# Kernel optimization log

Hardware: AMD Instinct MI355X
Metric: run time of the kernel (lower is better)

## Reference

```python
import jax, jax.numpy as jnp
import numpy as np

N, T = 1024, 32
D_FEAT, GATE_START, GATE_END = 158, 158, 221
D_MODEL = 256
T_NHEAD, S_NHEAD = 4, 2
BETA = 5.0
LN_EPS = 1e-5


def _ln(x, g, b):
    mu = jnp.mean(x, axis=-1, keepdims=True)
    var = jnp.mean(jnp.square(x - mu), axis=-1, keepdims=True)
    return (x - mu) * jax.lax.rsqrt(var + LN_EPS) * g + b


def _pos_enc(t, d):
    pos = jnp.arange(t, dtype=jnp.float32)[:, None]
    div = jnp.exp(jnp.arange(0, d, 2, dtype=jnp.float32) * (-np.log(10000.0) / d))
    pe = jnp.zeros((t, d), dtype=jnp.float32)
    pe = pe.at[:, 0::2].set(jnp.sin(pos * div))
    pe = pe.at[:, 1::2].set(jnp.cos(pos * div))
    return pe


def _mha(xn, qw, kw, vw, nhead, temperature):
    # xn: [B, S, D] (already layer-normed); attention over axis S
    B, S, D = xn.shape
    dh = D // nhead
    q = (xn @ qw.T).reshape(B, S, nhead, dh)
    k = (xn @ kw.T).reshape(B, S, nhead, dh)
    v = (xn @ vw.T).reshape(B, S, nhead, dh)
    scores = jnp.einsum('bshd,bthd->bhst', q, k) / temperature
    a = jax.nn.softmax(scores, axis=-1)
    return jnp.einsum('bhst,bthd->bshd', a, v).reshape(B, S, D)


def _block(x, qw, kw, vw, n1g, n1b, n2g, n2b, f1w, f1b, f2w, f2b, nhead, temperature):
    xn = _ln(x, n1g, n1b)
    xt = xn + _mha(xn, qw, kw, vw, nhead, temperature)
    xt = _ln(xt, n2g, n2b)
    ffn = jnp.maximum(xt @ f1w.T + f1b, 0.0) @ f2w.T + f2b
    return xt + ffn


def _forward(x, gate_w, gate_b, proj_w, proj_b,
             tq, tk, tv, tn1g, tn1b, tn2g, tn2b, tf1w, tf1b, tf2w, tf2b,
             sq, sk, sv, sn1g, sn1b, sn2g, sn2b, sf1w, sf1b, sf2w, sf2b,
             temp_w, out_w, out_b):
    src = x[:, :, :GATE_START]                     # [N, T, d_feat]
    gate_in = x[:, -1, GATE_START:GATE_END]        # [N, d_gate]
    gate = D_FEAT * jax.nn.softmax((gate_in @ gate_w.T + gate_b) / BETA, axis=-1)
    src = src * gate[:, None, :]
    z = src @ proj_w.T + proj_b                    # [N, T, d_model]
    z = z + _pos_enc(z.shape[1], D_MODEL)
    # TAttention: attend over time, unscaled scores (temperature=1)
    z = _block(z, tq, tk, tv, tn1g, tn1b, tn2g, tn2b, tf1w, tf1b, tf2w, tf2b,
               T_NHEAD, 1.0)
    # SAttention: attend over stocks, temperature = sqrt(d_model/nhead)
    zs = _block(z.swapaxes(0, 1), sq, sk, sv, sn1g, sn1b, sn2g, sn2b,
                sf1w, sf1b, sf2w, sf2b, S_NHEAD, float(np.sqrt(D_MODEL / S_NHEAD)))
    z = zs.swapaxes(0, 1)                          # [N, T, d_model]
    # TemporalAttention pooling
    h = z @ temp_w.T
    lam = jax.nn.softmax(jnp.einsum('ntd,nd->nt', h, h[:, -1, :]), axis=1)
    pooled = jnp.einsum('nt,ntd->nd', lam, z)
    return (pooled @ out_w.T + out_b).squeeze(-1)  # [N]


def setup_inputs() -> dict:
    key = jax.random.key(0)
    ks = iter(jax.random.split(key, 32))
    s = 0.02
    d, f, g = D_MODEL, D_FEAT, GATE_END - GATE_START
    inp = {
        'x': jax.random.normal(next(ks), (N, T, GATE_END), dtype=jnp.float32),
        'gate_w': jax.random.normal(next(ks), (f, g)) * s,
        'gate_b': jnp.zeros((f,)),
        'proj_w': jax.random.normal(next(ks), (d, f)) * s,
        'proj_b': jnp.zeros((d,)),
        'tq': jax.random.normal(next(ks), (d, d)) * s,
        'tk': jax.random.normal(next(ks), (d, d)) * s,
        'tv': jax.random.normal(next(ks), (d, d)) * s,
        'tn1g': jnp.ones((d,)), 'tn1b': jnp.zeros((d,)),
        'tn2g': jnp.ones((d,)), 'tn2b': jnp.zeros((d,)),
        'tf1w': jax.random.normal(next(ks), (d, d)) * s, 'tf1b': jnp.zeros((d,)),
        'tf2w': jax.random.normal(next(ks), (d, d)) * s, 'tf2b': jnp.zeros((d,)),
        'sq': jax.random.normal(next(ks), (d, d)) * s,
        'sk': jax.random.normal(next(ks), (d, d)) * s,
        'sv': jax.random.normal(next(ks), (d, d)) * s,
        'sn1g': jnp.ones((d,)), 'sn1b': jnp.zeros((d,)),
        'sn2g': jnp.ones((d,)), 'sn2b': jnp.zeros((d,)),
        'sf1w': jax.random.normal(next(ks), (d, d)) * s, 'sf1b': jnp.zeros((d,)),
        'sf2w': jax.random.normal(next(ks), (d, d)) * s, 'sf2b': jnp.zeros((d,)),
        'temp_w': jax.random.normal(next(ks), (d, d)) * s,
        'out_w': jax.random.normal(next(ks), (1, d)) * s,
        'out_b': jnp.zeros((1,)),
    }
    return {k: v.astype(jnp.float32) for k, v in inp.items()}


def reference(x, gate_w, gate_b, proj_w, proj_b,
              tq, tk, tv, tn1g, tn1b, tn2g, tn2b, tf1w, tf1b, tf2w, tf2b,
              sq, sk, sv, sn1g, sn1b, sn2g, sn2b, sf1w, sf1b, sf2w, sf2b,
              temp_w, out_w, out_b):
    return _forward(x, gate_w, gate_b, proj_w, proj_b,
                    tq, tk, tv, tn1g, tn1b, tn2g, tn2b, tf1w, tf1b, tf2w, tf2b,
                    sq, sk, sv, sn1g, sn1b, sn2g, sn2b, sf1w, sf1b, sf2w, sf2b,
                    temp_w, out_w, out_b)
```

## Files before the change

kernel.cpp:

```cpp
#include <hip/hip_runtime.h>
#include <math.h>

#define NB   1024
#define TSEQ 32
#define DM   256
#define DF   158
#define GDIM 63
#define XROW 221

typedef unsigned short u16;
typedef __attribute__((ext_vector_type(8))) __bf16 bf16x8;
typedef __attribute__((ext_vector_type(4))) float f32x4;
#define MFMA16(a,b,c) __builtin_amdgcn_mfma_f32_16x16x32_bf16(a,b,c,0,0,0)

#define MODE_PROJ 0
#define MODE_QKVT 1
#define MODE_QKVS 2
#define MODE_TEMP 3

__device__ __forceinline__ u16 f2bf(float f){
  union { float f; unsigned int u; } c; c.f = f;
  unsigned int u = c.u;
  u += 0x7fffu + ((u >> 16) & 1u);
  return (u16)(u >> 16);
}

__device__ __forceinline__ void ln_rows32(float* buf, int stride,
                                          const float* __restrict__ g,
                                          const float* __restrict__ b,
                                          int tid)
{
  const int s = tid >> 3, j = tid & 7;
  float* row = buf + s * stride;
  float sum = 0.f, sq = 0.f;
  #pragma unroll
  for (int k = 0; k < DM; k += 8){
    float v = row[k + j];
    sum += v; sq += v * v;
  }
  #pragma unroll
  for (int o = 1; o < 8; o <<= 1){
    sum += __shfl_xor(sum, o);
    sq  += __shfl_xor(sq, o);
  }
  const float mu  = sum * (1.f / DM);
  const float var = sq * (1.f / DM) - mu * mu;
  const float rs  = rsqrtf(var + 1e-5f);
  #pragma unroll
  for (int k = 0; k < DM; k += 8){
    float v = row[k + j];
    row[k + j] = (v - mu) * rs * g[k + j] + b[k + j];
  }
}

#define WB_TOT 770048

__global__ __launch_bounds__(256) void kConvAll(
    const float* __restrict__ tq, const float* __restrict__ tk, const float* __restrict__ tv,
    const float* __restrict__ sq, const float* __restrict__ sk, const float* __restrict__ sv,
    const float* __restrict__ tf1, const float* __restrict__ tf2,
    const float* __restrict__ sf1, const float* __restrict__ sf2,
    const float* __restrict__ tw, const float* __restrict__ pw,
    u16* __restrict__ WB)
{
  int i = blockIdx.x * 256 + threadIdx.x;
  if (i >= WB_TOT) return;
  if (i < 720896){
    int j = i >> 16, o = i & 65535;
    const float* s;
    switch (j){
      case 0: s = tq; break;  case 1: s = tk; break;  case 2: s = tv; break;
      case 3: s = sq; break;  case 4: s = sk; break;  case 5: s = sv; break;
      case 6: s = tf1; break; case 7: s = tf2; break;
      case 8: s = sf1; break; case 9: s = sf2; break;
      default: s = tw; break;
    }
    WB[i] = f2bf(s[o]);
  } else {
    int k = i - 720896;
    int row = k / 192, col = k - row * 192;
    WB[i] = (col < DF) ? f2bf(pw[row * DF + col]) : (u16)0;
  }
}


__global__ __launch_bounds__(256) void kGateSrc(
    const float* __restrict__ x,
    const float* __restrict__ gate_w, const float* __restrict__ gate_b,
    u16* __restrict__ SRC)
{
  __shared__ float s_gate[DF];
  __shared__ float s_gi[GDIM];
  const int tid = threadIdx.x;
  const int n = blockIdx.x;

  if (tid < GDIM) s_gi[tid] = x[(n * TSEQ + (TSEQ - 1)) * XROW + DF + tid];
  __syncthreads();
  float logit = 0.f;
  if (tid < DF){
    logit = gate_b[tid];
    const float* __restrict__ wr = gate_w + tid * GDIM;
    for (int g = 0; g < GDIM; ++g) logit += s_gi[g] * wr[g];
    logit *= 0.2f;
    s_gate[tid] = logit;
  }
  __syncthreads();
  {
    float mx = -1e30f;
    for (int f = 0; f < DF; ++f) mx = fmaxf(mx, s_gate[f]);
    float sm = 0.f;
    for (int f = 0; f < DF; ++f) sm += __expf(s_gate[f] - mx);
    __syncthreads();
    if (tid < DF) s_gate[tid] = (float)DF * __expf(logit - mx) / sm;
  }
  __syncthreads();

  for (int e = tid; e < TSEQ * 192; e += 256){
    int t = e / 192, f = e - t * 192;
    float v = 0.f;
    if (f < DF) v = x[(n * TSEQ + t) * XROW + f] * s_gate[f];
    SRC[(size_t)(n * TSEQ + t) * 192 + f] = f2bf(v);
  }
}


__global__ __launch_bounds__(256) void gemm_bf16(
    const u16* __restrict__ A, const u16* __restrict__ B,
    const int K, const int mode,
    const float* __restrict__ bias, const float* __restrict__ resid,
    float* __restrict__ outf,
    u16* __restrict__ ob0, u16* __restrict__ ob1, u16* __restrict__ ob2)
{
  __shared__ alignas(16) u16 sA[128 * 64];
  __shared__ alignas(16) u16 sB[128 * 64];
  const int tid = threadIdx.x;
  const int wv = tid >> 6, lane = tid & 63;
  const int wr = wv >> 1, wc = wv & 1;
  const int quad = lane >> 4, lc = lane & 15;
  const int m0 = blockIdx.x * 128, n0 = blockIdx.y * 128;

  const u16* srcA[4]; const u16* srcB[4];
  int dst[4];
  #pragma unroll
  for (int i = 0; i < 4; ++i){
    int c = tid + i * 256;
    int row = c >> 3, blk = c & 7;
    srcA[i] = A + (size_t)(m0 + row) * K + blk * 8;
    srcB[i] = B + (size_t)(n0 + row) * K + blk * 8;
    dst[i] = row * 64 + (blk ^ (row & 7)) * 8;
  }

  f32x4 acc[4][4];
  #pragma unroll
  for (int i = 0; i < 4; ++i)
    #pragma unroll
    for (int j = 0; j < 4; ++j) acc[i][j] = (f32x4){0.f,0.f,0.f,0.f};

  for (int kt = 0; kt < K; kt += 64){
    __syncthreads();
    #pragma unroll
    for (int i = 0; i < 4; ++i){
      *reinterpret_cast<uint4*>(&sA[dst[i]]) = *reinterpret_cast<const uint4*>(srcA[i] + kt);
      *reinterpret_cast<uint4*>(&sB[dst[i]]) = *reinterpret_cast<const uint4*>(srcB[i] + kt);
    }
    __syncthreads();
    #pragma unroll
    for (int kc = 0; kc < 2; ++kc){
      const int sw = ((kc * 4 + quad) ^ (lc & 7)) * 8;
      bf16x8 a[4], b[4];
      #pragma unroll
      for (int i = 0; i < 4; ++i){
        a[i] = *reinterpret_cast<const bf16x8*>(&sA[(wr * 64 + i * 16 + lc) * 64 + sw]);
        b[i] = *reinterpret_cast<const bf16x8*>(&sB[(wc * 64 + i * 16 + lc) * 64 + sw]);
      }
      #pragma unroll
      for (int i = 0; i < 4; ++i)
        #pragma unroll
        for (int j = 0; j < 4; ++j)
          acc[i][j] = MFMA16(a[i], b[j], acc[i][j]);
    }
  }

  const int rb = wr * 64 + quad * 4;
  const int cb = wc * 64 + lc;

  if (mode == MODE_PROJ){
    #pragma unroll
    for (int i = 0; i < 4; ++i)
      #pragma unroll
      for (int r = 0; r < 4; ++r){
        int row = m0 + rb + i * 16 + r;
        float ft = (float)(row & 31);
        #pragma unroll
        for (int j = 0; j < 4; ++j){
          int col = n0 + cb + j * 16;
          float div = __expf((float)(col & ~1) * -0.035977892f);
          float ang = ft * div;
          float pe = (col & 1) ? __cosf(ang) : __sinf(ang);
          outf[(size_t)row * 256 + col] = acc[i][j][r] + bias[col] + pe;
        }
      }
  } else if (mode == MODE_QKVT){
    #pragma unroll
    for (int i = 0; i < 4; ++i)
      #pragma unroll
      for (int r = 0; r < 4; ++r){
        int row = m0 + rb + i * 16 + r;
        #pragma unroll
        for (int j = 0; j < 4; ++j){
          int col = n0 + cb + j * 16;
          int sel = col >> 8, c = col & 255;
          u16 v = f2bf(acc[i][j][r]);
          if (sel == 0)      ob0[(size_t)row * 256 + c] = v;
          else if (sel == 1) ob1[(size_t)row * 256 + c] = v;
          else {
            int h = c >> 6, dd = c & 63;
            ob2[(((size_t)(row >> 5) * 4 + h) * 64 + dd) * 32 + (row & 31)] = v;
          }
        }
      }
  } else if (mode == MODE_QKVS){
    #pragma unroll
    for (int i = 0; i < 4; ++i)
      #pragma unroll
      for (int r = 0; r < 4; ++r){
        int row = m0 + rb + i * 16 + r;
        int n = row >> 5, t = row & 31;
        #pragma unroll
        for (int j = 0; j < 4; ++j){
          int col = n0 + cb + j * 16;
          int sel = col >> 8, c = col & 255;
          u16 v = f2bf(acc[i][j][r]);
          if (sel == 0)      ob0[((size_t)t * NB + n) * 256 + c] = v;
          else if (sel == 1) ob1[((size_t)t * NB + n) * 256 + c] = v;
          else {
            int h = c >> 7, dd = c & 127;
            ob2[(((size_t)t * 2 + h) * 128 + dd) * NB + n] = v;
          }
        }
      }
  } else {
    #pragma unroll
    for (int i = 0; i < 4; ++i)
      #pragma unroll
      for (int r = 0; r < 4; ++r){
        int row = m0 + rb + i * 16 + r;
        #pragma unroll
        for (int j = 0; j < 4; ++j){
          int col = n0 + cb + j * 16;
          outf[(size_t)row * 256 + col] = acc[i][j][r];
        }
      }
  }
}


__global__ __launch_bounds__(512) void kFFN(
    const float* __restrict__ X,
    const float* __restrict__ lg, const float* __restrict__ lb,
    const u16* __restrict__ w1, const float* __restrict__ b1,
    const u16* __restrict__ w2, const float* __restrict__ b2,
    float* __restrict__ outf, u16* __restrict__ obdual)
{
  __shared__ alignas(16) u16 sAB[24576];
  __shared__ alignas(16) u16 s_h1[128 * 256];
  __shared__ float s_mu[128], s_rs[128];
  __shared__ float s_lg[256], s_lb[256], s_b1[256], s_b2[256];

  const int tid = threadIdx.x;
  const int wv = tid >> 6, lane = tid & 63;
  const int quad = lane >> 4, lc = lane & 15;
  const int m0 = blockIdx.x * 128;
  const int m0w = (wv >> 1) * 32;
  const int n0w = (wv & 1) * 128;
  u16* sA = sAB;
  u16* sB = sAB + 8192;

  if (tid < 256){
    s_lg[tid] = lg[tid]; s_lb[tid] = lb[tid];
    s_b1[tid] = b1[tid]; s_b2[tid] = b2[tid];
  }

  {
    const int row = tid >> 2, j = tid & 3;
    const float4* xr = reinterpret_cast<const float4*>(X + (size_t)(m0 + row) * 256);
    float sum = 0.f, sq = 0.f;
    #pragma unroll
    for (int k = 0; k < 16; ++k){
      float4 v = xr[j + 4 * k];
      sum += v.x + v.y + v.z + v.w;
      sq  += v.x*v.x + v.y*v.y + v.z*v.z + v.w*v.w;
    }
    sum += __shfl_xor(sum, 1); sq += __shfl_xor(sq, 1);
    sum += __shfl_xor(sum, 2); sq += __shfl_xor(sq, 2);
    if (j == 0){
      float mu = sum * (1.f / 256.f);
      s_mu[row] = mu;
      s_rs[row] = rsqrtf(sq * (1.f / 256.f) - mu * mu + 1e-5f);
    }
  }
  __syncthreads();

  f32x4 acc[2][8];
  #pragma unroll
  for (int mt = 0; mt < 2; ++mt)
    #pragma unroll
    for (int j = 0; j < 8; ++j) acc[mt][j] = (f32x4){0.f,0.f,0.f,0.f};

  for (int kt = 0; kt < 4; ++kt){
    __syncthreads();
    {
      const int row = tid >> 2, c0 = (tid & 3) * 16;
      const float mu = s_mu[row], rs = s_rs[row];
      const float* xp = X + (size_t)(m0 + row) * 256 + kt * 64 + c0;
      u16 v16[16];
      #pragma unroll
      for (int k = 0; k < 4; ++k){
        float4 v = *reinterpret_cast<const float4*>(xp + 4 * k);
        int col = kt * 64 + c0 + 4 * k;
        v16[4*k+0] = f2bf((v.x - mu) * rs * s_lg[col+0] + s_lb[col+0]);
        v16[4*k+1] = f2bf((v.y - mu) * rs * s_lg[col+1] + s_lb[col+1]);
        v16[4*k+2] = f2bf((v.z - mu) * rs * s_lg[col+2] + s_lb[col+2]);
        v16[4*k+3] = f2bf((v.w - mu) * rs * s_lg[col+3] + s_lb[col+3]);
      }
      int b0 = c0 >> 3;
      *reinterpret_cast<uint4*>(&sA[row * 64 + ((b0    ) ^ (row & 7)) * 8]) = *reinterpret_cast<uint4*>(&v16[0]);
      *reinterpret_cast<uint4*>(&sA[row * 64 + ((b0 + 1) ^ (row & 7)) * 8]) = *reinterpret_cast<uint4*>(&v16[8]);
    }
    #pragma unroll
    for (int i = 0; i < 4; ++i){
      int c = tid + i * 512;
      int row = c >> 3, blk = c & 7;
      *reinterpret_cast<uint4*>(&sB[row * 64 + (blk ^ (row & 7)) * 8]) =
        *reinterpret_cast<const uint4*>(w1 + (size_t)row * 256 + kt * 64 + blk * 8);
    }
    __syncthreads();
    #pragma unroll
    for (int kc = 0; kc < 2; ++kc){
      const int sw = ((kc * 4 + quad) ^ (lc & 7)) * 8;
      bf16x8 a[2], b[8];
      #pragma unroll
      for (int mt = 0; mt < 2; ++mt)
        a[mt] = *reinterpret_cast<const bf16x8*>(&sA[(m0w + mt * 16 + lc) * 64 + sw]);
      #pragma unroll
      for (int j = 0; j < 8; ++j)
        b[j] = *reinterpret_cast<const bf16x8*>(&sB[(n0w + j * 16 + lc) * 64 + sw]);
      #pragma unroll
      for (int mt = 0; mt < 2; ++mt)
        #pragma unroll
        for (int j = 0; j < 8; ++j)
          acc[mt][j] = MFMA16(a[mt], b[j], acc[mt][j]);
    }
  }
  __syncthreads();

  #pragma unroll
  for (int mt = 0; mt < 2; ++mt)
    #pragma unroll
    for (int r = 0; r < 4; ++r){
      int row = m0w + mt * 16 + quad * 4 + r;
      #pragma unroll
      for (int j = 0; j < 8; ++j){
        int col = n0w + j * 16 + lc;
        u16 v = f2bf(fmaxf(acc[mt][j][r] + s_b1[col], 0.f));
        s_h1[row * 256 + (((col >> 3) ^ (row & 31)) << 3) + (col & 7)] = v;
      }
    }

  #pragma unroll
  for (int mt = 0; mt < 2; ++mt)
    #pragma unroll
    for (int j = 0; j < 8; ++j) acc[mt][j] = (f32x4){0.f,0.f,0.f,0.f};

  for (int kt = 0; kt < 4; ++kt){
    __syncthreads();
    #pragma unroll
    for (int i = 0; i < 4; ++i){
      int c = tid + i * 512;
      int row = c >> 3, blk = c & 7;
      *reinterpret_cast<uint4*>(&sAB[row * 64 + (blk ^ (row & 7)) * 8]) =
        *reinterpret_cast<const uint4*>(w2 + (size_t)row * 256 + kt * 64 + blk * 8);
    }
    __syncthreads();
    #pragma unroll
    for (int kc = 0; kc < 2; ++kc){
      const int sw = ((kc * 4 + quad) ^ (lc & 7)) * 8;
      bf16x8 a[2], b[8];
      #pragma unroll
      for (int mt = 0; mt < 2; ++mt){
        int row = m0w + mt * 16 + lc;
        int cb = kt * 8 + kc * 4 + quad;
        a[mt] = *reinterpret_cast<const bf16x8*>(
            &s_h1[row * 256 + ((cb ^ (row & 31)) << 3)]);
      }
      #pragma unroll
      for (int j = 0; j < 8; ++j)
        b[j] = *reinterpret_cast<const bf16x8*>(&sAB[(n0w + j * 16 + lc) * 64 + sw]);
      #pragma unroll
      for (int mt = 0; mt < 2; ++mt)
        #pragma unroll
        for (int j = 0; j < 8; ++j)
          acc[mt][j] = MFMA16(a[mt], b[j], acc[mt][j]);
    }
  }

  #pragma unroll
  for (int mt = 0; mt < 2; ++mt)
    #pragma unroll
    for (int r = 0; r < 4; ++r){
      int rowl = m0w + mt * 16 + quad * 4 + r;
      const float mu = s_mu[rowl], rs = s_rs[rowl];
      size_t base = (size_t)(m0 + rowl) * 256;
      #pragma unroll
      for (int j = 0; j < 8; ++j){
        int col = n0w + j * 16 + lc;
        float xn = (X[base + col] - mu) * rs * s_lg[col] + s_lb[col];
        float v = acc[mt][j][r] + s_b2[col] + xn;
        outf[base + col] = v;
        if (obdual) obdual[base + col] = f2bf(v);
      }
    }
}


__global__ __launch_bounds__(256) void kLN(
    const float* __restrict__ X, const float* __restrict__ g,
    const float* __restrict__ b,
    u16* __restrict__ Xb, float* __restrict__ Xf)
{
  __shared__ float s_z[32 * DM];
  const int tid = threadIdx.x;
  const size_t base = (size_t)blockIdx.x * (32 * DM);
  for (int e = tid; e < 32 * DM; e += 256) s_z[e] = X[base + e];
  __syncthreads();
  ln_rows32(s_z, DM, g, b, tid);
  __syncthreads();
  for (int e = tid; e < 32 * DM; e += 256){
    float v = s_z[e];
    Xb[base + e] = f2bf(v);
    Xf[base + e] = v;
  }
}


__global__ __launch_bounds__(256) void kAttnT(
    const u16* __restrict__ Qt, const u16* __restrict__ Kt,
    const u16* __restrict__ VtT, const float* __restrict__ XN1f,
    float* __restrict__ X2)
{
  __shared__ alignas(16) u16 sQ[4][32 * 72];
  __shared__ alignas(16) u16 sK[4][32 * 72];
  __shared__ alignas(16) u16 sV[4][64 * 40];
  __shared__ alignas(16) u16 sP[4][32 * 40];

  const int tid = threadIdx.x;
  const int wv = tid >> 6, lane = tid & 63;
  const int quad = lane >> 4, lc = lane & 15;
  const int n = blockIdx.x;
  const int h = wv;
  const f32x4 zero4 = {0.f, 0.f, 0.f, 0.f};

  #pragma unroll
  for (int i = 0; i < 4; ++i){
    int c = lane + 64 * i;
    int row = c >> 3, blk = c & 7;
    *reinterpret_cast<uint4*>(&sQ[wv][row * 72 + blk * 8]) =
      *reinterpret_cast<const uint4*>(&Qt[((size_t)n * 32 + row) * 256 + h * 64 + blk * 8]);
    *reinterpret_cast<uint4*>(&sK[wv][row * 72 + blk * 8]) =
      *reinterpret_cast<const uint4*>(&Kt[((size_t)n * 32 + row) * 256 + h * 64 + blk * 8]);
    int rv = c >> 2, bv = c & 3;
    *reinterpret_cast<uint4*>(&sV[wv][rv * 40 + bv * 8]) =
      *reinterpret_cast<const uint4*>(&VtT[(((size_t)n * 4 + h) * 64 + rv) * 32 + bv * 8]);
  }
  __syncthreads();

  f32x4 s[2][2];
  #pragma unroll
  for (int mt = 0; mt < 2; ++mt)
    #pragma unroll
    for (int ct = 0; ct < 2; ++ct) s[mt][ct] = zero4;
  #pragma unroll
  for (int kc = 0; kc < 2; ++kc){
    bf16x8 aq[2], bk[2];
    #pragma unroll
    for (int mt = 0; mt < 2; ++mt)
      aq[mt] = *reinterpret_cast<const bf16x8*>(&sQ[wv][(mt * 16 + lc) * 72 + kc * 32 + quad * 8]);
    #pragma unroll
    for (int ct = 0; ct < 2; ++ct)
      bk[ct] = *reinterpret_cast<const bf16x8*>(&sK[wv][(ct * 16 + lc) * 72 + kc * 32 + quad * 8]);
    #pragma unroll
    for (int mt = 0; mt < 2; ++mt)
      #pragma unroll
      for (int ct = 0; ct < 2; ++ct)
        s[mt][ct] = MFMA16(aq[mt], bk[ct], s[mt][ct]);
  }

  #pragma unroll
  for (int mt = 0; mt < 2; ++mt){
    #pragma unroll
    for (int r = 0; r < 4; ++r){
      float v0 = s[mt][0][r], v1 = s[mt][1][r];
      float mx = fmaxf(v0, v1);
      #pragma unroll
      for (int msk = 1; msk < 16; msk <<= 1) mx = fmaxf(mx, __shfl_xor(mx, msk));
      float p0 = __expf(v0 - mx), p1 = __expf(v1 - mx);
      float sm = p0 + p1;
      #pragma unroll
      for (int msk = 1; msk < 16; msk <<= 1) sm += __shfl_xor(sm, msk);
      float inv = 1.f / sm;
      sP[wv][(mt * 16 + quad * 4 + r) * 40 + lc]      = f2bf(p0 * inv);
      sP[wv][(mt * 16 + quad * 4 + r) * 40 + lc + 16] = f2bf(p1 * inv);
    }
  }
  __syncthreads();

  #pragma unroll
  for (int mt = 0; mt < 2; ++mt){
    bf16x8 ap = *reinterpret_cast<const bf16x8*>(&sP[wv][(mt * 16 + lc) * 40 + quad * 8]);
    #pragma unroll
    for (int ct = 0; ct < 4; ++ct){
      bf16x8 bv = *reinterpret_cast<const bf16x8*>(&sV[wv][(ct * 16 + lc) * 40 + quad * 8]);
      f32x4 o = MFMA16(ap, bv, zero4);
      #pragma unroll
      for (int r = 0; r < 4; ++r){
        int t = mt * 16 + quad * 4 + r;
        size_t idx = ((size_t)n * 32 + t) * 256 + h * 64 + ct * 16 + lc;
        X2[idx] = XN1f[idx] + o[r];
      }
    }
  }
}


__global__ __launch_bounds__(256) void kB2_flash_mfma(
    const u16* __restrict__ Qh, const u16* __restrict__ Kh,
    const u16* __restrict__ VT, const float* __restrict__ XNs,
    float* __restrict__ XT)
{
  __shared__ alignas(16) u16 s_k[64 * 136];
  __shared__ alignas(16) u16 s_vt[128 * 72];
  __shared__ alignas(16) u16 s_p[4][32 * 72];

  const int tid = threadIdx.x;
  const int wv = tid >> 6, lane = tid & 63;
  const int quad = lane >> 4, lc = lane & 15;
  const int n0 = blockIdx.x * 128;
  const int h = blockIdx.y, t = blockIdx.z;
  const float c_exp2 = 0.12752887f;
  const int qb = n0 + wv * 32;

  bf16x8 qf[2][4];
  #pragma unroll
  for (int mt = 0; mt < 2; ++mt){
    const u16* qp = Qh + ((size_t)(t * NB + qb + mt * 16 + lc)) * DM + h * 128 + quad * 8;
    #pragma unroll
    for (int kc = 0; kc < 4; ++kc)
      qf[mt][kc] = *reinterpret_cast<const bf16x8*>(qp + kc * 32);
  }

  f32x4 o[2][8];
  #pragma unroll
  for (int mt = 0; mt < 2; ++mt)
    #pragma unroll
    for (int f = 0; f < 8; ++f) o[mt][f] = (f32x4){0.f, 0.f, 0.f, 0.f};
  float l_acc[2][4] = {{0.f,0.f,0.f,0.f},{0.f,0.f,0.f,0.f}};

  const u16* kbase  = Kh + (size_t)t * NB * DM + h * 128;
  const u16* vtbase = VT + (size_t)(t * 2 + h) * 128 * NB;
  u16* pw = s_p[wv];

  for (int j0 = 0; j0 < NB; j0 += 64){
    __syncthreads();
    #pragma unroll
    for (int it = 0; it < 4; ++it){
      int c = tid + it * 256;
      int row = c >> 4, part = c & 15;
      *reinterpret_cast<uint4*>(&s_k[row * 136 + part * 8]) =
        *reinterpret_cast<const uint4*>(kbase + (size_t)(j0 + row) * DM + part * 8);
      int rv = c >> 3, pv = c & 7;
      *reinterpret_cast<uint4*>(&s_vt[rv * 72 + pv * 8]) =
        *reinterpret_cast<const uint4*>(vtbase + (size_t)rv * NB + j0 + pv * 8);
    }
    __syncthreads();

    f32x4 s[2][4];
    #pragma unroll
    for (int mt = 0; mt < 2; ++mt)
      #pragma unroll
      for (int nt = 0; nt < 4; ++nt) s[mt][nt] = (f32x4){0.f,0.f,0.f,0.f};
    #pragma unroll
    for (int kc = 0; kc < 4; ++kc){
      #pragma unroll
      for (int nt = 0; nt < 4; ++nt){
        bf16x8 bk = *reinterpret_cast<const bf16x8*>(
            &s_k[(lc + 16 * nt) * 136 + kc * 32 + quad * 8]);
        #pragma unroll
        for (int mt = 0; mt < 2; ++mt)
          s[mt][nt] = MFMA16(qf[mt][kc], bk, s[mt][nt]);
      }
    }

    #pragma unroll
    for (int mt = 0; mt < 2; ++mt)
      #pragma unroll
      for (int nt = 0; nt < 4; ++nt)
        #pragma unroll
        for (int r = 0; r < 4; ++r){
          float p = exp2f(s[mt][nt][r] * c_exp2);
          l_acc[mt][r] += p;
          pw[(mt * 16 + quad * 4 + r) * 72 + lc + 16 * nt] = f2bf(p);
        }

    bf16x8 ap[2][2];
    #pragma unroll
    for (int mt = 0; mt < 2; ++mt){
      ap[mt][0] = *reinterpret_cast<const bf16x8*>(&pw[(mt * 16 + lc) * 72 + quad * 8]);
      ap[mt][1] = *reinterpret_cast<const bf16x8*>(&pw[(mt * 16 + lc) * 72 + 32 + quad * 8]);
    }
    #pragma unroll
    for (int f = 0; f < 8; ++f){
      bf16x8 bv0 = *reinterpret_cast<const bf16x8*>(&s_vt[(lc + 16 * f) * 72 + quad * 8]);
      bf16x8 bv1 = *reinterpret_cast<const bf16x8*>(&s_vt[(lc + 16 * f) * 72 + 32 + quad * 8]);
      #pragma unroll
      for (int mt = 0; mt < 2; ++mt){
        o[mt][f] = MFMA16(ap[mt][0], bv0, o[mt][f]);
        o[mt][f] = MFMA16(ap[mt][1], bv1, o[mt][f]);
      }
    }
  }

  #pragma unroll
  for (int mt = 0; mt < 2; ++mt)
    #pragma unroll
    for (int r = 0; r < 4; ++r){
      #pragma unroll
      for (int msk = 1; msk < 16; msk <<= 1)
        l_acc[mt][r] += __shfl_xor(l_acc[mt][r], msk);
    }

  #pragma unroll
  for (int mt = 0; mt < 2; ++mt)
    #pragma unroll
    for (int r = 0; r < 4; ++r){
      float linv = 1.f / l_acc[mt][r];
      int row = qb + mt * 16 + quad * 4 + r;
      size_t xnb = ((size_t)row * TSEQ + t) * DM + h * 128 + lc;
      size_t xtb = ((size_t)t * NB + row) * DM + h * 128 + lc;
      #pragma unroll
      for (int f = 0; f < 8; ++f)
        XT[xtb + f * 16] = XNs[xnb + f * 16] + o[mt][f][r] * linv;
    }
}


__global__ __launch_bounds__(256) void kC_pool(
    const float* __restrict__ Ht, const float* __restrict__ ZS,
    const float* __restrict__ out_w, const float* __restrict__ out_b,
    float* __restrict__ out)
{
  __shared__ float s_z[32 * DM];
  __shared__ float s_h[32 * 260];
  __shared__ float s_sc[32];
  __shared__ float s_red[4];
  const int tid = threadIdx.x;
  const int n = blockIdx.x;

  for (int e = tid; e < 32 * DM; e += 256){
    int i = e >> 8, dd = e & 255;
    s_h[i * 260 + dd] = Ht[((size_t)i * NB + n) * DM + dd];
    s_z[e]            = ZS[((size_t)i * NB + n) * DM + dd];
  }
  __syncthreads();

  {
    const int s = tid >> 3, j = tid & 7;
    float acc = 0.f;
    #pragma unroll
    for (int k = 0; k < DM; k += 8) acc += s_h[s * 260 + k + j] * s_h[31 * 260 + k + j];
    #pragma unroll
    for (int o = 1; o < 8; o <<= 1) acc += __shfl_xor(acc, o);
    if (j == 0) s_sc[s] = acc;
  }
  __syncthreads();

  float mx = -1e30f;
  #pragma unroll
  for (int s = 0; s < 32; ++s) mx = fmaxf(mx, s_sc[s]);
  float sm = 0.f;
  #pragma unroll
  for (int s = 0; s < 32; ++s) sm += __expf(s_sc[s] - mx);
  const float inv = 1.f / sm;

  const int d = tid;
  float pooled = 0.f;
  #pragma unroll
  for (int s = 0; s < 32; ++s) pooled += __expf(s_sc[s] - mx) * inv * s_z[s * DM + d];

  float val = pooled * out_w[d];
  #pragma unroll
  for (int o = 1; o < 64; o <<= 1) val += __shfl_xor(val, o);
  if ((tid & 63) == 0) s_red[tid >> 6] = val;
  __syncthreads();
  if (tid == 0) out[n] = s_red[0] + s_red[1] + s_red[2] + s_red[3] + out_b[0];
}


extern "C" void kernel_launch(void* const* d_in, const int* in_sizes, int n_in,
                              void* d_out, int out_size, void* d_ws, size_t ws_size,
                              hipStream_t stream)
{
  const float* x      = (const float*)d_in[0];
  const float* gate_w = (const float*)d_in[1];
  const float* gate_b = (const float*)d_in[2];
  const float* proj_w = (const float*)d_in[3];
  const float* proj_b = (const float*)d_in[4];
  const float* tq   = (const float*)d_in[5];
  const float* tk   = (const float*)d_in[6];
  const float* tv   = (const float*)d_in[7];
  const float* tn1g = (const float*)d_in[8];
  const float* tn1b = (const float*)d_in[9];
  const float* tn2g = (const float*)d_in[10];
  const float* tn2b = (const float*)d_in[11];
  const float* tf1w = (const float*)d_in[12];
  const float* tf1b = (const float*)d_in[13];
  const float* tf2w = (const float*)d_in[14];
  const float* tf2b = (const float*)d_in[15];
  const float* sq   = (const float*)d_in[16];
  const float* sk   = (const float*)d_in[17];
  const float* sv   = (const float*)d_in[18];
  const float* sn1g = (const float*)d_in[19];
  const float* sn1b = (const float*)d_in[20];
  const float* sn2g = (const float*)d_in[21];
  const float* sn2b = (const float*)d_in[22];
  const float* sf1w = (const float*)d_in[23];
  const float* sf1b = (const float*)d_in[24];
  const float* sf2w = (const float*)d_in[25];
  const float* sf2b = (const float*)d_in[26];
  const float* temp_w = (const float*)d_in[27];
  const float* out_w  = (const float*)d_in[28];
  const float* out_b  = (const float*)d_in[29];

  float* W = (float*)d_ws;
  const size_t F = (size_t)NB * TSEQ * DM;

  float* Z  = W;
  float* XF = W + F;
  u16* U0 = (u16*)(W + 2 * F);
  u16* U1 = (u16*)(W + 2 * F) + F;
  u16* U2 = (u16*)(W + 3 * F);
  u16* U3 = (u16*)(W + 3 * F) + F;
  u16* SRC = (u16*)(W + 4 * F);
  u16* WB  = (u16*)(W + 4 * F + 3145728 + 4096);

  kConvAll<<<(WB_TOT + 255) / 256, 256, 0, stream>>>(
      tq, tk, tv, sq, sk, sv, tf1w, tf2w, sf1w, sf2w, temp_w, proj_w, WB);
  kGateSrc<<<NB, 256, 0, stream>>>(x, gate_w, gate_b, SRC);
  gemm_bf16<<<dim3(256, 2), 256, 0, stream>>>(SRC, WB + 720896, 192, MODE_PROJ,
      proj_b, nullptr, Z, nullptr, nullptr, nullptr);
  kLN<<<NB, 256, 0, stream>>>(Z, tn1g, tn1b, U0, XF);
  gemm_bf16<<<dim3(256, 6), 256, 0, stream>>>(U0, WB, 256, MODE_QKVT,
      nullptr, nullptr, nullptr, U1, U2, U3);
  kAttnT<<<NB, 256, 0, stream>>>(U1, U2, U3, XF, Z);
  kFFN<<<256, 512, 0, stream>>>(Z, tn2g, tn2b, WB + 393216, tf1b,
      WB + 458752, tf2b, Z, nullptr);
  kLN<<<NB, 256, 0, stream>>>(Z, sn1g, sn1b, U2, XF);
  gemm_bf16<<<dim3(256, 6), 256, 0, stream>>>(U2, WB + 196608, 256, MODE_QKVS,
      nullptr, nullptr, nullptr, U3, U1, U0);
  kB2_flash_mfma<<<dim3(NB / 128, 2, TSEQ), 256, 0, stream>>>(U3, U1, U0, XF, Z);
  kFFN<<<256, 512, 0, stream>>>(Z, sn2g, sn2b, WB + 524288, sf1b,
      WB + 589824, sf2b, Z, U0);
  gemm_bf16<<<dim3(256, 2), 256, 0, stream>>>(U0, WB + 655360, 256, MODE_TEMP,
      nullptr, nullptr, XF, nullptr, nullptr, nullptr);
  kC_pool<<<NB, 256, 0, stream>>>(XF, Z, out_w, out_b, (float*)d_out);
}
```

Measured before the change: 534.0 us.

## Fuse LayerNorm into QKV GEMM A-load and use direct global-to-LDS loads

Removes the two standalone LayerNorm kernels and folds their work into the QKV GEMMs. Each block computes per-row mean and rstd from fp32 input, normalizes and converts the A tile to bf16 while staging it into LDS, and the n0==0 column blocks write the fp32 normalized copy that later stages read. B tiles, and A tiles in the non-LN modes, are now staged with the global_load_lds builtin instead of register round-trips. This saves two launches and a bf16 intermediate round-trip to memory. In exchange, the six column blocks of each row tile each recompute the row statistics and reread the fp32 input, which is twice the size of bf16.

```diff
diff --git a/kernel.cpp b/kernel.cpp
--- a/kernel.cpp
+++ b/kernel.cpp
@@ -25,32 +25,16 @@
   return (u16)(u >> 16);
 }
 
-__device__ __forceinline__ void ln_rows32(float* buf, int stride,
-                                          const float* __restrict__ g,
-                                          const float* __restrict__ b,
-                                          int tid)
-{
-  const int s = tid >> 3, j = tid & 7;
-  float* row = buf + s * stride;
-  float sum = 0.f, sq = 0.f;
-  #pragma unroll
-  for (int k = 0; k < DM; k += 8){
-    float v = row[k + j];
-    sum += v; sq += v * v;
-  }
-  #pragma unroll
-  for (int o = 1; o < 8; o <<= 1){
-    sum += __shfl_xor(sum, o);
-    sq  += __shfl_xor(sq, o);
-  }
-  const float mu  = sum * (1.f / DM);
-  const float var = sq * (1.f / DM) - mu * mu;
-  const float rs  = rsqrtf(var + 1e-5f);
-  #pragma unroll
-  for (int k = 0; k < DM; k += 8){
-    float v = row[k + j];
-    row[k + j] = (v - mu) * rs * g[k + j] + b[k + j];
-  }
+__device__ __forceinline__ void gl2lds16(const u16* g, u16* lds_wave_base, int lane){
+#if __has_builtin(__builtin_amdgcn_global_load_lds)
+  __builtin_amdgcn_global_load_lds(
+      (const __attribute__((address_space(1))) unsigned int*)g,
+      (__attribute__((address_space(3))) unsigned int*)lds_wave_base,
+      16, 0, 0);
+#else
+  *reinterpret_cast<uint4*>(lds_wave_base + lane * 8) =
+      *reinterpret_cast<const uint4*>(g);
+#endif
 }
 
 #define WB_TOT 770048
@@ -126,28 +110,45 @@
 
 __global__ __launch_bounds__(256) void gemm_bf16(
     const u16* __restrict__ A, const u16* __restrict__ B,
+    const float* __restrict__ Afp,
     const int K, const int mode,
-    const float* __restrict__ bias, const float* __restrict__ resid,
+    const float* __restrict__ bias,
+    const float* __restrict__ lg, const float* __restrict__ lb,
+    float* __restrict__ xf,
     float* __restrict__ outf,
     u16* __restrict__ ob0, u16* __restrict__ ob1, u16* __restrict__ ob2)
 {
   __shared__ alignas(16) u16 sA[128 * 64];
   __shared__ alignas(16) u16 sB[128 * 64];
+  __shared__ float s_mu[128], s_rs[128];
+  __shared__ float s_lg[256], s_lb[256];
+
   const int tid = threadIdx.x;
   const int wv = tid >> 6, lane = tid & 63;
   const int wr = wv >> 1, wc = wv & 1;
   const int quad = lane >> 4, lc = lane & 15;
   const int m0 = blockIdx.x * 128, n0 = blockIdx.y * 128;
-
-  const u16* srcA[4]; const u16* srcB[4];
-  int dst[4];
-  #pragma unroll
-  for (int i = 0; i < 4; ++i){
-    int c = tid + i * 256;
-    int row = c >> 3, blk = c & 7;
-    srcA[i] = A + (size_t)(m0 + row) * K + blk * 8;
-    srcB[i] = B + (size_t)(n0 + row) * K + blk * 8;
-    dst[i] = row * 64 + (blk ^ (row & 7)) * 8;
+  const bool lnA = (mode == MODE_QKVT || mode == MODE_QKVS);
+
+  if (lnA){
+    s_lg[tid] = lg[tid];
+    s_lb[tid] = lb[tid];
+    const int row = tid >> 1, j = tid & 1;
+    const float4* xr = reinterpret_cast<const float4*>(Afp + (size_t)(m0 + row) * 256);
+    float sum = 0.f, sq = 0.f;
+    #pragma unroll
+    for (int k = 0; k < 32; ++k){
+      float4 v = xr[j + 2 * k];
+      sum += v.x + v.y + v.z + v.w;
+      sq  += v.x*v.x + v.y*v.y + v.z*v.z + v.w*v.w;
+    }
+    sum += __shfl_xor(sum, 1); sq += __shfl_xor(sq, 1);
+    if (j == 0){
+      float mu = sum * (1.f / 256.f);
+      s_mu[row] = mu;
+      s_rs[row] = rsqrtf(sq * (1.f / 256.f) - mu * mu + 1e-5f);
+    }
+    __syncthreads();
   }
 
   f32x4 acc[4][4];
@@ -159,9 +160,49 @@
   for (int kt = 0; kt < K; kt += 64){
     __syncthreads();
     #pragma unroll
-    for (int i = 0; i < 4; ++i){
-      *reinterpret_cast<uint4*>(&sA[dst[i]]) = *reinterpret_cast<const uint4*>(srcA[i] + kt);
-      *reinterpret_cast<uint4*>(&sB[dst[i]]) = *reinterpret_cast<const uint4*>(srcB[i] + kt);
+    for (int j = 0; j < 4; ++j){
+      int c = wv * 64 + lane + j * 256;
+      int row = c >> 3, blk = c & 7;
+      gl2lds16(B + (size_t)(n0 + row) * K + kt + ((blk ^ (row & 7)) * 8),
+               &sB[(wv * 64 + j * 256) * 8], lane);
+    }
+    if (lnA){
+      const int row = tid >> 1, c0 = (tid & 1) * 32;
+      const float mu = s_mu[row], rs = s_rs[row];
+      const float* xp = Afp + (size_t)(m0 + row) * 256 + kt + c0;
+      u16 v16[32];
+      float4 lnv[8];
+      #pragma unroll
+      for (int k = 0; k < 8; ++k){
+        float4 v = *reinterpret_cast<const float4*>(xp + 4 * k);
+        int col = kt + c0 + 4 * k;
+        lnv[k].x = (v.x - mu) * rs * s_lg[col+0] + s_lb[col+0];
+        lnv[k].y = (v.y - mu) * rs * s_lg[col+1] + s_lb[col+1];
+        lnv[k].z = (v.z - mu) * rs * s_lg[col+2] + s_lb[col+2];
+        lnv[k].w = (v.w - mu) * rs * s_lg[col+3] + s_lb[col+3];
+        v16[4*k+0] = f2bf(lnv[k].x);
+        v16[4*k+1] = f2bf(lnv[k].y);
+        v16[4*k+2] = f2bf(lnv[k].z);
+        v16[4*k+3] = f2bf(lnv[k].w);
+      }
+      const int b0 = c0 >> 3;
+      #pragma unroll
+      for (int s = 0; s < 4; ++s)
+        *reinterpret_cast<uint4*>(&sA[row * 64 + (((b0 + s) ^ (row & 7)) * 8)]) =
+            *reinterpret_cast<uint4*>(&v16[8 * s]);
+      if (xf && n0 == 0){
+        float4* xo = reinterpret_cast<float4*>(xf + (size_t)(m0 + row) * 256 + kt + c0);
+        #pragma unroll
+        for (int k = 0; k < 8; ++k) xo[k] = lnv[k];
+      }
+    } else {
+      #pragma unroll
+      for (int j = 0; j < 4; ++j){
+        int c = wv * 64 + lane + j * 256;
+        int row = c >> 3, blk = c & 7;
+        gl2lds16(A + (size_t)(m0 + row) * K + kt + ((blk ^ (row & 7)) * 8),
+                 &sA[(wv * 64 + j * 256) * 8], lane);
+      }
     }
     __syncthreads();
     #pragma unroll
@@ -420,26 +461,6 @@
         if (obdual) obdual[base + col] = f2bf(v);
       }
     }
-}
-
-
-__global__ __launch_bounds__(256) void kLN(
-    const float* __restrict__ X, const float* __restrict__ g,
-    const float* __restrict__ b,
-    u16* __restrict__ Xb, float* __restrict__ Xf)
-{
-  __shared__ float s_z[32 * DM];
-  const int tid = threadIdx.x;
-  const size_t base = (size_t)blockIdx.x * (32 * DM);
-  for (int e = tid; e < 32 * DM; e += 256) s_z[e] = X[base + e];
-  __syncthreads();
-  ln_rows32(s_z, DM, g, b, tid);
-  __syncthreads();
-  for (int e = tid; e < 32 * DM; e += 256){
-    float v = s_z[e];
-    Xb[base + e] = f2bf(v);
-    Xf[base + e] = v;
-  }
 }
 
 
@@ -755,21 +776,19 @@
   kConvAll<<<(WB_TOT + 255) / 256, 256, 0, stream>>>(
       tq, tk, tv, sq, sk, sv, tf1w, tf2w, sf1w, sf2w, temp_w, proj_w, WB);
   kGateSrc<<<NB, 256, 0, stream>>>(x, gate_w, gate_b, SRC);
-  gemm_bf16<<<dim3(256, 2), 256, 0, stream>>>(SRC, WB + 720896, 192, MODE_PROJ,
-      proj_b, nullptr, Z, nullptr, nullptr, nullptr);
-  kLN<<<NB, 256, 0, stream>>>(Z, tn1g, tn1b, U0, XF);
-  gemm_bf16<<<dim3(256, 6), 256, 0, stream>>>(U0, WB, 256, MODE_QKVT,
-      nullptr, nullptr, nullptr, U1, U2, U3);
+  gemm_bf16<<<dim3(256, 2), 256, 0, stream>>>(SRC, WB + 720896, nullptr, 192, MODE_PROJ,
+      proj_b, nullptr, nullptr, nullptr, Z, nullptr, nullptr, nullptr);
+  gemm_bf16<<<dim3(256, 6), 256, 0, stream>>>(nullptr, WB, Z, 256, MODE_QKVT,
+      nullptr, tn1g, tn1b, XF, nullptr, U1, U2, U3);
   kAttnT<<<NB, 256, 0, stream>>>(U1, U2, U3, XF, Z);
   kFFN<<<256, 512, 0, stream>>>(Z, tn2g, tn2b, WB + 393216, tf1b,
       WB + 458752, tf2b, Z, nullptr);
-  kLN<<<NB, 256, 0, stream>>>(Z, sn1g, sn1b, U2, XF);
-  gemm_bf16<<<dim3(256, 6), 256, 0, stream>>>(U2, WB + 196608, 256, MODE_QKVS,
-      nullptr, nullptr, nullptr, U3, U1, U0);
+  gemm_bf16<<<dim3(256, 6), 256, 0, stream>>>(nullptr, WB + 196608, Z, 256, MODE_QKVS,
+      nullptr, sn1g, sn1b, XF, nullptr, U3, U1, U0);
   kB2_flash_mfma<<<dim3(NB / 128, 2, TSEQ), 256, 0, stream>>>(U3, U1, U0, XF, Z);
   kFFN<<<256, 512, 0, stream>>>(Z, sn2g, sn2b, WB + 524288, sf1b,
       WB + 589824, sf2b, Z, U0);
-  gemm_bf16<<<dim3(256, 2), 256, 0, stream>>>(U0, WB + 655360, 256, MODE_TEMP,
-      nullptr, nullptr, XF, nullptr, nullptr, nullptr);
+  gemm_bf16<<<dim3(256, 2), 256, 0, stream>>>(U0, WB + 655360, nullptr, 256, MODE_TEMP,
+      nullptr, nullptr, nullptr, nullptr, XF, nullptr, nullptr, nullptr);
   kC_pool<<<NB, 256, 0, stream>>>(XF, Z, out_w, out_b, (float*)d_out);
 }
```

Result: slower. 585.1 us (+9.6%).

## Load GEMM tiles directly into LDS and regroup S-attention QKV tiles by time step

Applied to the files above, without the earlier changes.

The GEMM tile loads now use global_load_lds, which copies global memory straight into LDS without passing through registers. The XOR swizzle is applied on the global source address so the LDS layout stays the same. In MODE_QKVS, each block now covers 128 stocks at a single time step, so the scattered time-major output stores become contiguous. The flash attention grid is remapped so that t and h vary fastest, which changes the block order for cache locality. This also drops the unused resid parameter and moves kLN within the file, and relies on the builtin being available, with a register-path fallback otherwise.

```diff
diff --git a/kernel.cpp b/kernel.cpp
--- a/kernel.cpp
+++ b/kernel.cpp
@@ -23,6 +23,18 @@
   unsigned int u = c.u;
   u += 0x7fffu + ((u >> 16) & 1u);
   return (u16)(u >> 16);
+}
+
+__device__ __forceinline__ void gl2lds16(const u16* g, u16* lds_wave_base, int lane){
+#if __has_builtin(__builtin_amdgcn_global_load_lds)
+  __builtin_amdgcn_global_load_lds(
+      (const __attribute__((address_space(1))) unsigned int*)g,
+      (__attribute__((address_space(3))) unsigned int*)lds_wave_base,
+      16, 0, 0);
+#else
+  *reinterpret_cast<uint4*>(lds_wave_base + lane * 8) =
+      *reinterpret_cast<const uint4*>(g);
+#endif
 }
 
 __device__ __forceinline__ void ln_rows32(float* buf, int stride,
@@ -127,7 +139,7 @@
 __global__ __launch_bounds__(256) void gemm_bf16(
     const u16* __restrict__ A, const u16* __restrict__ B,
     const int K, const int mode,
-    const float* __restrict__ bias, const float* __restrict__ resid,
+    const float* __restrict__ bias,
     float* __restrict__ outf,
     u16* __restrict__ ob0, u16* __restrict__ ob1, u16* __restrict__ ob2)
 {
@@ -137,18 +149,11 @@
   const int wv = tid >> 6, lane = tid & 63;
   const int wr = wv >> 1, wc = wv & 1;
   const int quad = lane >> 4, lc = lane & 15;
-  const int m0 = blockIdx.x * 128, n0 = blockIdx.y * 128;
-
-  const u16* srcA[4]; const u16* srcB[4];
-  int dst[4];
-  #pragma unroll
-  for (int i = 0; i < 4; ++i){
-    int c = tid + i * 256;
-    int row = c >> 3, blk = c & 7;
-    srcA[i] = A + (size_t)(m0 + row) * K + blk * 8;
-    srcB[i] = B + (size_t)(n0 + row) * K + blk * 8;
-    dst[i] = row * 64 + (blk ^ (row & 7)) * 8;
-  }
+  const int n0 = blockIdx.y * 128;
+  const bool tmaj = (mode == MODE_QKVS);
+  const int tt = tmaj ? (blockIdx.x & 31) : 0;
+  const int nb = tmaj ? (blockIdx.x >> 5) : 0;
+  const int m0 = tmaj ? 0 : blockIdx.x * 128;
 
   f32x4 acc[4][4];
   #pragma unroll
@@ -159,9 +164,14 @@
   for (int kt = 0; kt < K; kt += 64){
     __syncthreads();
     #pragma unroll
-    for (int i = 0; i < 4; ++i){
-      *reinterpret_cast<uint4*>(&sA[dst[i]]) = *reinterpret_cast<const uint4*>(srcA[i] + kt);
-      *reinterpret_cast<uint4*>(&sB[dst[i]]) = *reinterpret_cast<const uint4*>(srcB[i] + kt);
+    for (int j = 0; j < 4; ++j){
+      int c = wv * 64 + lane + j * 256;
+      int row = c >> 3, blk = c & 7;
+      int arow = tmaj ? ((nb * 128 + row) * 32 + tt) : (m0 + row);
+      gl2lds16(A + (size_t)arow * K + kt + ((blk ^ (row & 7)) * 8),
+               &sA[(wv * 64 + j * 256) * 8], lane);
+      gl2lds16(B + (size_t)(n0 + row) * K + kt + ((blk ^ (row & 7)) * 8),
+               &sB[(wv * 64 + j * 256) * 8], lane);
     }
     __syncthreads();
     #pragma unroll
@@ -224,18 +234,18 @@
     for (int i = 0; i < 4; ++i)
       #pragma unroll
       for (int r = 0; r < 4; ++r){
-        int row = m0 + rb + i * 16 + r;
-        int n = row >> 5, t = row & 31;
+        int rl = rb + i * 16 + r;
+        int n = nb * 128 + rl;
         #pragma unroll
         for (int j = 0; j < 4; ++j){
           int col = n0 + cb + j * 16;
           int sel = col >> 8, c = col & 255;
           u16 v = f2bf(acc[i][j][r]);
-          if (sel == 0)      ob0[((size_t)t * NB + n) * 256 + c] = v;
-          else if (sel == 1) ob1[((size_t)t * NB + n) * 256 + c] = v;
+          if (sel == 0)      ob0[((size_t)tt * NB + n) * 256 + c] = v;
+          else if (sel == 1) ob1[((size_t)tt * NB + n) * 256 + c] = v;
           else {
             int h = c >> 7, dd = c & 127;
-            ob2[(((size_t)t * 2 + h) * 128 + dd) * NB + n] = v;
+            ob2[(((size_t)tt * 2 + h) * 128 + dd) * NB + n] = v;
           }
         }
       }
@@ -251,6 +261,26 @@
           outf[(size_t)row * 256 + col] = acc[i][j][r];
         }
       }
+  }
+}
+
+
+__global__ __launch_bounds__(256) void kLN(
+    const float* __restrict__ X, const float* __restrict__ g,
+    const float* __restrict__ b,
+    u16* __restrict__ Xb, float* __restrict__ Xf)
+{
+  __shared__ float s_z[32 * DM];
+  const int tid = threadIdx.x;
+  const size_t base = (size_t)blockIdx.x * (32 * DM);
+  for (int e = tid; e < 32 * DM; e += 256) s_z[e] = X[base + e];
+  __syncthreads();
+  ln_rows32(s_z, DM, g, b, tid);
+  __syncthreads();
+  for (int e = tid; e < 32 * DM; e += 256){
+    float v = s_z[e];
+    Xb[base + e] = f2bf(v);
+    Xf[base + e] = v;
   }
 }
 
@@ -420,26 +450,6 @@
         if (obdual) obdual[base + col] = f2bf(v);
       }
     }
-}
-
-
-__global__ __launch_bounds__(256) void kLN(
-    const float* __restrict__ X, const float* __restrict__ g,
-    const float* __restrict__ b,
-    u16* __restrict__ Xb, float* __restrict__ Xf)
-{
-  __shared__ float s_z[32 * DM];
-  const int tid = threadIdx.x;
-  const size_t base = (size_t)blockIdx.x * (32 * DM);
-  for (int e = tid; e < 32 * DM; e += 256) s_z[e] = X[base + e];
-  __syncthreads();
-  ln_rows32(s_z, DM, g, b, tid);
-  __syncthreads();
-  for (int e = tid; e < 32 * DM; e += 256){
-    float v = s_z[e];
-    Xb[base + e] = f2bf(v);
-    Xf[base + e] = v;
-  }
 }
 
 
@@ -544,8 +554,8 @@
   const int tid = threadIdx.x;
   const int wv = tid >> 6, lane = tid & 63;
   const int quad = lane >> 4, lc = lane & 15;
-  const int n0 = blockIdx.x * 128;
-  const int h = blockIdx.y, t = blockIdx.z;
+  const int t = blockIdx.x >> 1, h = blockIdx.x & 1;
+  const int n0 = blockIdx.y * 128;
   const float c_exp2 = 0.12752887f;
   const int qb = n0 + wv * 32;
 
@@ -756,20 +766,20 @@
       tq, tk, tv, sq, sk, sv, tf1w, tf2w, sf1w, sf2w, temp_w, proj_w, WB);
   kGateSrc<<<NB, 256, 0, stream>>>(x, gate_w, gate_b, SRC);
   gemm_bf16<<<dim3(256, 2), 256, 0, stream>>>(SRC, WB + 720896, 192, MODE_PROJ,
-      proj_b, nullptr, Z, nullptr, nullptr, nullptr);
+      proj_b, Z, nullptr, nullptr, nullptr);
   kLN<<<NB, 256, 0, stream>>>(Z, tn1g, tn1b, U0, XF);
   gemm_bf16<<<dim3(256, 6), 256, 0, stream>>>(U0, WB, 256, MODE_QKVT,
-      nullptr, nullptr, nullptr, U1, U2, U3);
+      nullptr, nullptr, U1, U2, U3);
   kAttnT<<<NB, 256, 0, stream>>>(U1, U2, U3, XF, Z);
   kFFN<<<256, 512, 0, stream>>>(Z, tn2g, tn2b, WB + 393216, tf1b,
       WB + 458752, tf2b, Z, nullptr);
   kLN<<<NB, 256, 0, stream>>>(Z, sn1g, sn1b, U2, XF);
   gemm_bf16<<<dim3(256, 6), 256, 0, stream>>>(U2, WB + 196608, 256, MODE_QKVS,
-      nullptr, nullptr, nullptr, U3, U1, U0);
-  kB2_flash_mfma<<<dim3(NB / 128, 2, TSEQ), 256, 0, stream>>>(U3, U1, U0, XF, Z);
+      nullptr, nullptr, U3, U1, U0);
+  kB2_flash_mfma<<<dim3(64, 8), 256, 0, stream>>>(U3, U1, U0, XF, Z);
   kFFN<<<256, 512, 0, stream>>>(Z, sn2g, sn2b, WB + 524288, sf1b,
       WB + 589824, sf2b, Z, U0);
   gemm_bf16<<<dim3(256, 2), 256, 0, stream>>>(U0, WB + 655360, 256, MODE_TEMP,
-      nullptr, nullptr, XF, nullptr, nullptr, nullptr);
+      nullptr, XF, nullptr, nullptr, nullptr);
   kC_pool<<<NB, 256, 0, stream>>>(XF, Z, out_w, out_b, (float*)d_out);
 }
```

New measurement: 497.7 us. 6.8% less time.
